# Optimization experiments

Measured on AMD Instinct MI355X. Metric: run time of the kernel, lower is better.

Reference implementation:

```python
import jax, jax.numpy as jnp
import numpy as np

INPUT_DIM = 561
NUM_CLASSES = 6
CAP_DIM = 8
NUM_CAPS = 4


def setup_inputs() -> dict:
    key = jax.random.key(0)
    ks = jax.random.split(key, 20)
    def lin(kw, kb, out_d, in_d):
        bound = 1.0 / np.sqrt(in_d)
        W = jax.random.uniform(kw, (out_d, in_d), jnp.float32, -bound, bound)
        b = jax.random.uniform(kb, (out_d,), jnp.float32, -bound, bound)
        return W, b
    x = jax.random.normal(ks[0], (65536, INPUT_DIM), jnp.float32)
    feature_weights = jnp.ones((INPUT_DIM,), jnp.float32)
    cap_W, cap_b = lin(ks[1], ks[2], NUM_CAPS * CAP_DIM, INPUT_DIM)
    q_W, q_b = lin(ks[3], ks[4], CAP_DIM, CAP_DIM)
    k_W, k_b = lin(ks[5], ks[6], CAP_DIM, CAP_DIM)
    v_W, v_b = lin(ks[7], ks[8], CAP_DIM, CAP_DIM)
    fc1_W, fc1_b = lin(ks[9], ks[10], 64, NUM_CAPS * CAP_DIM)
    fc2_W, fc2_b = lin(ks[11], ks[12], 64, 64)
    res_W, res_b = lin(ks[13], ks[14], 64, NUM_CAPS * CAP_DIM)
    out_W, out_b = lin(ks[15], ks[16], NUM_CLASSES, 64)
    return dict(x=x, feature_weights=feature_weights,
                cap_W=cap_W, cap_b=cap_b,
                q_W=q_W, q_b=q_b, k_W=k_W, k_b=k_b, v_W=v_W, v_b=v_b,
                fc1_W=fc1_W, fc1_b=fc1_b, fc2_W=fc2_W, fc2_b=fc2_b,
                res_W=res_W, res_b=res_b, out_W=out_W, out_b=out_b)


def reference(x, feature_weights, cap_W, cap_b, q_W, q_b, k_W, k_b, v_W, v_b,
              fc1_W, fc1_b, fc2_W, fc2_b, res_W, res_b, out_W, out_b):
    B = x.shape[0]
    xw = x * feature_weights
    caps = (xw @ cap_W.T + cap_b).reshape(B, NUM_CAPS, CAP_DIM)  # [B,4,8]
    Q = caps @ q_W.T + q_b
    K = caps @ k_W.T + k_b
    V = caps @ v_W.T + v_b
    scores = jnp.einsum('bqd,bkd->bqk', Q, K) / jnp.sqrt(jnp.float32(CAP_DIM))
    attn = jax.nn.softmax(scores, axis=-1)
    attended = jnp.einsum('bqk,bkd->bqd', attn, V)
    flat = attended.reshape(B, NUM_CAPS * CAP_DIM)
    res = jax.nn.relu(flat @ fc1_W.T + fc1_b)
    out = jax.nn.relu(res @ fc2_W.T + fc2_b + flat @ res_W.T + res_b)
    return out @ out_W.T + out_b
```

## Files before the change

### kernel.cpp

```cpp
#include <hip/hip_runtime.h>
#include <math.h>

#define INPUT_DIM 561
#define NCD 32

__global__ void prep_wt(const float* __restrict__ capW,
                        const float* __restrict__ fw,
                        float* __restrict__ Wt) {
    int idx = blockIdx.x * blockDim.x + threadIdx.x;
    if (idx < INPUT_DIM * NCD) {
        int k = idx >> 5;
        int c = idx & 31;
        Wt[idx] = capW[c * INPUT_DIM + k] * fw[k];
    }
}

__device__ __forceinline__ void stage16(const float* __restrict__ X,
                                        int r0, int k0, int w_s, int lane,
                                        float (*dst)[65]) {
    int kk = k0 + lane;
    if (kk > INPUT_DIM - 1) kk = INPUT_DIM - 1;
    #pragma unroll
    for (int i = 0; i < 16; ++i) {
        const int p = w_s * 16 + i;
        const float* g = X + (size_t)(r0 + p) * INPUT_DIM + kk;
        __builtin_amdgcn_global_load_lds(
            (const __attribute__((address_space(1))) void*)g,
            (__attribute__((address_space(3))) void*)&dst[p][0],
            4, 0, 0);
    }
}

__global__ void __launch_bounds__(256)
__attribute__((amdgpu_waves_per_eu(4, 4)))
caps_gemm(const float* __restrict__ X,
          const float* __restrict__ Wt,
          const float* __restrict__ cap_b,
          float* __restrict__ caps)
{
    __shared__ float smem[8448];
    float (*xb)[64][65]   = (float (*)[64][65])smem;
    float (*part)[64][33] = (float (*)[64][33])smem;

    const int tid = threadIdx.x;
    const int t   = tid & 63;
    const int w   = tid >> 6;
    const int w_s = __builtin_amdgcn_readfirstlane(w);
    const int r0  = blockIdx.x * 64;

    float acc[NCD];
    #pragma unroll
    for (int c = 0; c < NCD; ++c) acc[c] = 0.0f;

    stage16(X, r0, 0, w_s, t, xb[0]);

    const int tb = (w_s == 0) ? 0 : (13 + 12 * (w_s - 1));
    const int te = tb + ((w_s == 0) ? 13 : 12);

    int cur = 0;
    for (int ch = 0; ch < 9; ++ch) {
        asm volatile("s_waitcnt vmcnt(0)" ::: "memory");
        __syncthreads();
        const int k0 = ch * 64;
        if (ch < 8) stage16(X, r0, k0 + 64, w_s, t, xb[cur ^ 1]);

        if (ch < 8) {
            const int kb = w_s * 16;
            #pragma unroll 4
            for (int jj = 0; jj < 16; ++jj) {
                const int j = kb + jj;
                const float xv = xb[cur][t][j];
                const float* __restrict__ wrow = Wt + (size_t)(k0 + j) * NCD;
                #pragma unroll
                for (int c = 0; c < NCD; ++c)
                    acc[c] = fmaf(xv, wrow[c], acc[c]);
            }
        } else {
            for (int j = tb; j < te; ++j) {
                const float xv = xb[cur][t][j];
                const float* __restrict__ wrow = Wt + (size_t)(k0 + j) * NCD;
                #pragma unroll
                for (int c = 0; c < NCD; ++c)
                    acc[c] = fmaf(xv, wrow[c], acc[c]);
            }
        }
        cur ^= 1;
    }

    __syncthreads();
    #pragma unroll
    for (int c = 0; c < NCD; ++c) part[w][t][c] = acc[c];
    __syncthreads();
    if (w != 0) return;

    float4* __restrict__ crow = (float4*)(caps + (size_t)(r0 + t) * NCD);
    #pragma unroll
    for (int v = 0; v < 8; ++v) {
        float4 s;
        s.x = cap_b[4*v+0] + part[0][t][4*v+0] + part[1][t][4*v+0]
            + part[2][t][4*v+0] + part[3][t][4*v+0];
        s.y = cap_b[4*v+1] + part[0][t][4*v+1] + part[1][t][4*v+1]
            + part[2][t][4*v+1] + part[3][t][4*v+1];
        s.z = cap_b[4*v+2] + part[0][t][4*v+2] + part[1][t][4*v+2]
            + part[2][t][4*v+2] + part[3][t][4*v+2];
        s.w = cap_b[4*v+3] + part[0][t][4*v+3] + part[1][t][4*v+3]
            + part[2][t][4*v+3] + part[3][t][4*v+3];
        crow[v] = s;
    }
}

__device__ __forceinline__ void head_body(
    const float* __restrict__ acc,
    const float* __restrict__ qW, const float* __restrict__ qb,
    const float* __restrict__ kW, const float* __restrict__ kb,
    const float* __restrict__ vW, const float* __restrict__ vb,
    const float* __restrict__ fc1W, const float* __restrict__ fc1b,
    const float* __restrict__ fc2W, const float* __restrict__ fc2b,
    const float* __restrict__ resW, const float* __restrict__ resb,
    const float* __restrict__ outW, const float* __restrict__ outb,
    float* __restrict__ o)
{
    float Km[32], Vm[32];
    #pragma unroll
    for (int q = 0; q < 4; ++q) {
        #pragma unroll
        for (int d = 0; d < 8; ++d) {
            float ka = kb[d], va = vb[d];
            #pragma unroll
            for (int e = 0; e < 8; ++e) {
                ka = fmaf(acc[q * 8 + e], kW[d * 8 + e], ka);
                va = fmaf(acc[q * 8 + e], vW[d * 8 + e], va);
            }
            Km[q * 8 + d] = ka;
            Vm[q * 8 + d] = va;
        }
    }

    float flat[32];
    const float rs8 = 0.35355339059327373f;
    #pragma unroll
    for (int q = 0; q < 4; ++q) {
        float Q[8];
        #pragma unroll
        for (int d = 0; d < 8; ++d) {
            float a = qb[d];
            #pragma unroll
            for (int e = 0; e < 8; ++e)
                a = fmaf(acc[q * 8 + e], qW[d * 8 + e], a);
            Q[d] = a;
        }
        float sc[4];
        #pragma unroll
        for (int kq = 0; kq < 4; ++kq) {
            float a = 0.0f;
            #pragma unroll
            for (int d = 0; d < 8; ++d)
                a = fmaf(Q[d], Km[kq * 8 + d], a);
            sc[kq] = a * rs8;
        }
        const float m  = fmaxf(fmaxf(sc[0], sc[1]), fmaxf(sc[2], sc[3]));
        const float e0 = __expf(sc[0] - m);
        const float e1 = __expf(sc[1] - m);
        const float e2 = __expf(sc[2] - m);
        const float e3 = __expf(sc[3] - m);
        const float inv = 1.0f / (e0 + e1 + e2 + e3);
        #pragma unroll
        for (int d = 0; d < 8; ++d)
            flat[q * 8 + d] =
                (e0 * Vm[0 * 8 + d] + e1 * Vm[1 * 8 + d] +
                 e2 * Vm[2 * 8 + d] + e3 * Vm[3 * 8 + d]) * inv;
    }

    float res[64];
    #pragma unroll
    for (int j = 0; j < 64; ++j) {
        float a = fc1b[j];
        #pragma unroll
        for (int i = 0; i < 32; ++i)
            a = fmaf(flat[i], fc1W[j * 32 + i], a);
        res[j] = fmaxf(a, 0.0f);
    }

    #pragma unroll
    for (int p = 0; p < 6; ++p) o[p] = outb[p];
    for (int c = 0; c < 64; ++c) {
        float a = fc2b[c] + resb[c];
        #pragma unroll
        for (int j = 0; j < 64; ++j)
            a = fmaf(res[j], fc2W[c * 64 + j], a);
        #pragma unroll
        for (int i = 0; i < 32; ++i)
            a = fmaf(flat[i], resW[c * 32 + i], a);
        a = fmaxf(a, 0.0f);
        #pragma unroll
        for (int p = 0; p < 6; ++p)
            o[p] = fmaf(a, outW[p * 64 + c], o[p]);
    }
}

__global__ void __launch_bounds__(256)
__attribute__((amdgpu_waves_per_eu(1, 1)))
head_kernel(const float* __restrict__ caps,
            const float* __restrict__ qW, const float* __restrict__ qb,
            const float* __restrict__ kW, const float* __restrict__ kb,
            const float* __restrict__ vW, const float* __restrict__ vb,
            const float* __restrict__ fc1W, const float* __restrict__ fc1b,
            const float* __restrict__ fc2W, const float* __restrict__ fc2b,
            const float* __restrict__ resW, const float* __restrict__ resb,
            const float* __restrict__ outW, const float* __restrict__ outb,
            float* __restrict__ out)
{
    const int row = blockIdx.x * 256 + threadIdx.x;
    const float4* __restrict__ cp = (const float4*)(caps + (size_t)row * NCD);
    float acc[NCD];
    #pragma unroll
    for (int i = 0; i < 8; ++i) {
        const float4 v = cp[i];
        acc[4 * i + 0] = v.x; acc[4 * i + 1] = v.y;
        acc[4 * i + 2] = v.z; acc[4 * i + 3] = v.w;
    }
    float o[6];
    head_body(acc, qW, qb, kW, kb, vW, vb, fc1W, fc1b, fc2W, fc2b,
              resW, resb, outW, outb, o);
    #pragma unroll
    for (int p = 0; p < 6; ++p) out[row * 6 + p] = o[p];
}

__global__ void __launch_bounds__(256)
harcnet_fused(const float* __restrict__ X,
              const float* __restrict__ fw,
              const float* __restrict__ capW, const float* __restrict__ cap_b,
              const float* __restrict__ qW, const float* __restrict__ qb,
              const float* __restrict__ kW, const float* __restrict__ kb,
              const float* __restrict__ vW, const float* __restrict__ vb,
              const float* __restrict__ fc1W, const float* __restrict__ fc1b,
              const float* __restrict__ fc2W, const float* __restrict__ fc2b,
              const float* __restrict__ resW, const float* __restrict__ resb,
              const float* __restrict__ outW, const float* __restrict__ outb,
              float* __restrict__ out)
{
    __shared__ float part[4][64][33];
    const int t   = threadIdx.x & 63;
    const int w   = threadIdx.x >> 6;
    const int row = blockIdx.x * 64 + t;
    const float* __restrict__ Xrow = X + (size_t)row * INPUT_DIM;

    float acc[NCD];
    #pragma unroll
    for (int c = 0; c < NCD; ++c) acc[c] = 0.0f;

    const int kbeg = w * 141;
    const int kend = (kbeg + 141 < INPUT_DIM) ? kbeg + 141 : INPUT_DIM;
    for (int k = kbeg; k < kend; ++k) {
        const float xv = Xrow[k] * fw[k];
        #pragma unroll
        for (int c = 0; c < NCD; ++c)
            acc[c] = fmaf(xv, capW[c * INPUT_DIM + k], acc[c]);
    }

    #pragma unroll
    for (int c = 0; c < NCD; ++c) part[w][t][c] = acc[c];
    __syncthreads();
    if (w != 0) return;
    #pragma unroll
    for (int c = 0; c < NCD; ++c)
        acc[c] = cap_b[c] + part[0][t][c] + part[1][t][c]
                          + part[2][t][c] + part[3][t][c];
    float o[6];
    head_body(acc, qW, qb, kW, kb, vW, vb, fc1W, fc1b, fc2W, fc2b,
              resW, resb, outW, outb, o);
    #pragma unroll
    for (int p = 0; p < 6; ++p) out[row * 6 + p] = o[p];
}

extern "C" void kernel_launch(void* const* d_in, const int* in_sizes, int n_in,
                              void* d_out, int out_size, void* d_ws, size_t ws_size,
                              hipStream_t stream) {
    const float* X     = (const float*)d_in[0];
    const float* fw    = (const float*)d_in[1];
    const float* capW  = (const float*)d_in[2];
    const float* cap_b = (const float*)d_in[3];
    const float* qW    = (const float*)d_in[4];
    const float* qb    = (const float*)d_in[5];
    const float* kW    = (const float*)d_in[6];
    const float* kb    = (const float*)d_in[7];
    const float* vW    = (const float*)d_in[8];
    const float* vb    = (const float*)d_in[9];
    const float* fc1W  = (const float*)d_in[10];
    const float* fc1b  = (const float*)d_in[11];
    const float* fc2W  = (const float*)d_in[12];
    const float* fc2b  = (const float*)d_in[13];
    const float* resW  = (const float*)d_in[14];
    const float* resb  = (const float*)d_in[15];
    const float* outW  = (const float*)d_in[16];
    const float* outb  = (const float*)d_in[17];
    float* out = (float*)d_out;

    const int nrows = in_sizes[0] / INPUT_DIM;
    const size_t caps_off   = 73728;
    const size_t caps_bytes = (size_t)nrows * NCD * sizeof(float);

    float* Wt   = (float*)d_ws;
    float* caps = (float*)((char*)d_ws + caps_off);

    if (ws_size >= caps_off + caps_bytes) {
        prep_wt<<<(INPUT_DIM * NCD + 255) / 256, 256, 0, stream>>>(capW, fw, Wt);
        caps_gemm<<<nrows / 64, 256, 0, stream>>>(X, Wt, cap_b, caps);
        head_kernel<<<nrows / 256, 256, 0, stream>>>(
            caps, qW, qb, kW, kb, vW, vb, fc1W, fc1b, fc2W, fc2b,
            resW, resb, outW, outb, out);
    } else {
        harcnet_fused<<<nrows / 64, 256, 0, stream>>>(
            X, fw, capW, cap_b, qW, qb, kW, kb, vW, vb,
            fc1W, fc1b, fc2W, fc2b, resW, resb, outW, outb, out);
    }
}
```

Before: 382.7 us.

## Split head MLP across 4 threads per row with packed LDS weights

The head kernel now assigns four threads to each row. Each thread computes 16 of the fc1 outputs and 16 of the fc2 outputs, gathers the full fc1 result through shuffles, and the six output logits are reduced with xor shuffles. All head weights are packed into one workspace buffer by a new pack kernel and staged into LDS per block, and occupancy hints move from 1 to 3-4 waves per EU. This is meant to cut the per-thread register pressure and serial work of the previous one-row-per-thread head, which ran at one wave per EU. In exchange the attention part is recomputed redundantly by all four threads and an extra small kernel launch is added. The caps GEMM inner loop also preloads 16 LDS values before the FMA loop.

Result: faster. 332.6 us (-13.1%).

```diff
diff --git a/kernel.cpp b/kernel.cpp
--- a/kernel.cpp
+++ b/kernel.cpp
@@ -3,6 +3,22 @@
 
 #define INPUT_DIM 561
 #define NCD 32
+
+#define QW   0
+#define QB   64
+#define KW   72
+#define KB   136
+#define VW   144
+#define VB   208
+#define FC1W 216
+#define FC1B 2264
+#define FC2W 2328
+#define FC2B 6424
+#define RESW 6488
+#define RESB 8536
+#define OUTW 8600
+#define OUTB 8984
+#define HW_N 8990
 
 __global__ void prep_wt(const float* __restrict__ capW,
                         const float* __restrict__ fw,
@@ -13,6 +29,34 @@
         int c = idx & 31;
         Wt[idx] = capW[c * INPUT_DIM + k] * fw[k];
     }
+}
+
+__global__ void pack_hw(const float* __restrict__ qW, const float* __restrict__ qb,
+                        const float* __restrict__ kW, const float* __restrict__ kb,
+                        const float* __restrict__ vW, const float* __restrict__ vb,
+                        const float* __restrict__ fc1W, const float* __restrict__ fc1b,
+                        const float* __restrict__ fc2W, const float* __restrict__ fc2b,
+                        const float* __restrict__ resW, const float* __restrict__ resb,
+                        const float* __restrict__ outW, const float* __restrict__ outb,
+                        float* __restrict__ hw) {
+    int i = blockIdx.x * blockDim.x + threadIdx.x;
+    if (i >= HW_N) return;
+    float v;
+    if      (i < QB)   v = qW[i - QW];
+    else if (i < KW)   v = qb[i - QB];
+    else if (i < KB)   v = kW[i - KW];
+    else if (i < VW)   v = kb[i - KB];
+    else if (i < VB)   v = vW[i - VW];
+    else if (i < FC1W) v = vb[i - VB];
+    else if (i < FC1B) v = fc1W[i - FC1W];
+    else if (i < FC2W) v = fc1b[i - FC1B];
+    else if (i < FC2B) v = fc2W[i - FC2W];
+    else if (i < RESW) v = fc2b[i - FC2B];
+    else if (i < RESB) v = resW[i - RESW];
+    else if (i < OUTW) v = resb[i - RESB];
+    else if (i < OUTB) v = outW[i - OUTW];
+    else               v = outb[i - OUTB];
+    hw[i] = v;
 }
 
 __device__ __forceinline__ void stage16(const float* __restrict__ X,
@@ -66,14 +110,16 @@
 
         if (ch < 8) {
             const int kb = w_s * 16;
-            #pragma unroll 4
+            float xv[16];
+            #pragma unroll
+            for (int jj = 0; jj < 16; ++jj)
+                xv[jj] = xb[cur][t][kb + jj];
+            #pragma unroll
             for (int jj = 0; jj < 16; ++jj) {
-                const int j = kb + jj;
-                const float xv = xb[cur][t][j];
-                const float* __restrict__ wrow = Wt + (size_t)(k0 + j) * NCD;
+                const float* __restrict__ wrow = Wt + (size_t)(k0 + kb + jj) * NCD;
                 #pragma unroll
                 for (int c = 0; c < NCD; ++c)
-                    acc[c] = fmaf(xv, wrow[c], acc[c]);
+                    acc[c] = fmaf(xv[jj], wrow[c], acc[c]);
             }
         } else {
             for (int j = tb; j < te; ++j) {
@@ -109,30 +155,42 @@
     }
 }
 
-__device__ __forceinline__ void head_body(
-    const float* __restrict__ acc,
-    const float* __restrict__ qW, const float* __restrict__ qb,
-    const float* __restrict__ kW, const float* __restrict__ kb,
-    const float* __restrict__ vW, const float* __restrict__ vb,
-    const float* __restrict__ fc1W, const float* __restrict__ fc1b,
-    const float* __restrict__ fc2W, const float* __restrict__ fc2b,
-    const float* __restrict__ resW, const float* __restrict__ resb,
-    const float* __restrict__ outW, const float* __restrict__ outb,
-    float* __restrict__ o)
+__global__ void __launch_bounds__(256)
+__attribute__((amdgpu_waves_per_eu(3, 4)))
+head_kernel(const float* __restrict__ caps,
+            const float* __restrict__ hwg,
+            float* __restrict__ out)
 {
+    __shared__ float hw[HW_N];
+    const int tid = threadIdx.x;
+    for (int i = tid; i < HW_N; i += 256) hw[i] = hwg[i];
+    __syncthreads();
+
+    const int g    = tid & 3;
+    const int row  = blockIdx.x * 64 + (tid >> 2);
+    const int lane = tid & 63;
+
+    const float4* __restrict__ cp = (const float4*)(caps + (size_t)row * NCD);
+    float acc[NCD];
+    #pragma unroll
+    for (int i = 0; i < 8; ++i) {
+        const float4 v = cp[i];
+        acc[4*i+0] = v.x; acc[4*i+1] = v.y; acc[4*i+2] = v.z; acc[4*i+3] = v.w;
+    }
+
     float Km[32], Vm[32];
     #pragma unroll
     for (int q = 0; q < 4; ++q) {
         #pragma unroll
         for (int d = 0; d < 8; ++d) {
-            float ka = kb[d], va = vb[d];
+            float ka = hw[KB + d], va = hw[VB + d];
             #pragma unroll
             for (int e = 0; e < 8; ++e) {
-                ka = fmaf(acc[q * 8 + e], kW[d * 8 + e], ka);
-                va = fmaf(acc[q * 8 + e], vW[d * 8 + e], va);
+                ka = fmaf(acc[q*8+e], hw[KW + d*8+e], ka);
+                va = fmaf(acc[q*8+e], hw[VW + d*8+e], va);
             }
-            Km[q * 8 + d] = ka;
-            Vm[q * 8 + d] = va;
+            Km[q*8+d] = ka;
+            Vm[q*8+d] = va;
         }
     }
 
@@ -143,10 +201,10 @@
         float Q[8];
         #pragma unroll
         for (int d = 0; d < 8; ++d) {
-            float a = qb[d];
+            float a = hw[QB + d];
             #pragma unroll
             for (int e = 0; e < 8; ++e)
-                a = fmaf(acc[q * 8 + e], qW[d * 8 + e], a);
+                a = fmaf(acc[q*8+e], hw[QW + d*8+e], a);
             Q[d] = a;
         }
         float sc[4];
@@ -155,75 +213,70 @@
             float a = 0.0f;
             #pragma unroll
             for (int d = 0; d < 8; ++d)
-                a = fmaf(Q[d], Km[kq * 8 + d], a);
+                a = fmaf(Q[d], Km[kq*8+d], a);
             sc[kq] = a * rs8;
         }
         const float m  = fmaxf(fmaxf(sc[0], sc[1]), fmaxf(sc[2], sc[3]));
-        const float e0 = __expf(sc[0] - m);
-        const float e1 = __expf(sc[1] - m);
-        const float e2 = __expf(sc[2] - m);
-        const float e3 = __expf(sc[3] - m);
-        const float inv = 1.0f / (e0 + e1 + e2 + e3);
+        const float e0 = __expf(sc[0]-m), e1 = __expf(sc[1]-m);
+        const float e2 = __expf(sc[2]-m), e3 = __expf(sc[3]-m);
+        const float inv = 1.0f / (e0+e1+e2+e3);
         #pragma unroll
         for (int d = 0; d < 8; ++d)
-            flat[q * 8 + d] =
-                (e0 * Vm[0 * 8 + d] + e1 * Vm[1 * 8 + d] +
-                 e2 * Vm[2 * 8 + d] + e3 * Vm[3 * 8 + d]) * inv;
-    }
-
-    float res[64];
-    #pragma unroll
-    for (int j = 0; j < 64; ++j) {
-        float a = fc1b[j];
+            flat[q*8+d] = (e0*Vm[0*8+d] + e1*Vm[1*8+d] +
+                           e2*Vm[2*8+d] + e3*Vm[3*8+d]) * inv;
+    }
+
+    const int j0 = g * 16;
+    float res_[16];
+    #pragma unroll
+    for (int jj = 0; jj < 16; ++jj) {
+        const int j = j0 + jj;
+        float a = hw[FC1B + j];
         #pragma unroll
         for (int i = 0; i < 32; ++i)
-            a = fmaf(flat[i], fc1W[j * 32 + i], a);
-        res[j] = fmaxf(a, 0.0f);
-    }
-
-    #pragma unroll
-    for (int p = 0; p < 6; ++p) o[p] = outb[p];
-    for (int c = 0; c < 64; ++c) {
-        float a = fc2b[c] + resb[c];
+            a = fmaf(flat[i], hw[FC1W + j*32 + i], a);
+        res_[jj] = fmaxf(a, 0.0f);
+    }
+
+    float res_full[64];
+    const int lbase = lane & ~3;
+    #pragma unroll
+    for (int gg = 0; gg < 4; ++gg) {
+        #pragma unroll
+        for (int jj = 0; jj < 16; ++jj)
+            res_full[gg*16 + jj] = __shfl(res_[jj], lbase | gg, 64);
+    }
+
+    float o[6];
+    #pragma unroll
+    for (int p = 0; p < 6; ++p) o[p] = 0.0f;
+
+    #pragma unroll 2
+    for (int cc = 0; cc < 16; ++cc) {
+        const int c = j0 + cc;
+        float s = hw[FC2B + c] + hw[RESB + c];
         #pragma unroll
         for (int j = 0; j < 64; ++j)
-            a = fmaf(res[j], fc2W[c * 64 + j], a);
+            s = fmaf(res_full[j], hw[FC2W + c*64 + j], s);
         #pragma unroll
         for (int i = 0; i < 32; ++i)
-            a = fmaf(flat[i], resW[c * 32 + i], a);
-        a = fmaxf(a, 0.0f);
+            s = fmaf(flat[i], hw[RESW + c*32 + i], s);
+        s = fmaxf(s, 0.0f);
         #pragma unroll
         for (int p = 0; p < 6; ++p)
-            o[p] = fmaf(a, outW[p * 64 + c], o[p]);
-    }
-}
-
-__global__ void __launch_bounds__(256)
-__attribute__((amdgpu_waves_per_eu(1, 1)))
-head_kernel(const float* __restrict__ caps,
-            const float* __restrict__ qW, const float* __restrict__ qb,
-            const float* __restrict__ kW, const float* __restrict__ kb,
-            const float* __restrict__ vW, const float* __restrict__ vb,
-            const float* __restrict__ fc1W, const float* __restrict__ fc1b,
-            const float* __restrict__ fc2W, const float* __restrict__ fc2b,
-            const float* __restrict__ resW, const float* __restrict__ resb,
-            const float* __restrict__ outW, const float* __restrict__ outb,
-            float* __restrict__ out)
-{
-    const int row = blockIdx.x * 256 + threadIdx.x;
-    const float4* __restrict__ cp = (const float4*)(caps + (size_t)row * NCD);
-    float acc[NCD];
-    #pragma unroll
-    for (int i = 0; i < 8; ++i) {
-        const float4 v = cp[i];
-        acc[4 * i + 0] = v.x; acc[4 * i + 1] = v.y;
-        acc[4 * i + 2] = v.z; acc[4 * i + 3] = v.w;
-    }
-    float o[6];
-    head_body(acc, qW, qb, kW, kb, vW, vb, fc1W, fc1b, fc2W, fc2b,
-              resW, resb, outW, outb, o);
-    #pragma unroll
-    for (int p = 0; p < 6; ++p) out[row * 6 + p] = o[p];
+            o[p] = fmaf(s, hw[OUTW + p*64 + c], o[p]);
+    }
+
+    #pragma unroll
+    for (int p = 0; p < 6; ++p) {
+        o[p] += __shfl_xor(o[p], 1, 64);
+        o[p] += __shfl_xor(o[p], 2, 64);
+    }
+    if (g == 0) {
+        #pragma unroll
+        for (int p = 0; p < 6; ++p)
+            out[row*6 + p] = o[p] + hw[OUTB + p];
+    }
 }
 
 __global__ void __launch_bounds__(256)
@@ -266,11 +319,71 @@
     for (int c = 0; c < NCD; ++c)
         acc[c] = cap_b[c] + part[0][t][c] + part[1][t][c]
                           + part[2][t][c] + part[3][t][c];
+
+    float Km[32], Vm[32];
+    #pragma unroll
+    for (int q = 0; q < 4; ++q)
+        #pragma unroll
+        for (int d = 0; d < 8; ++d) {
+            float ka = kb[d], va = vb[d];
+            #pragma unroll
+            for (int e = 0; e < 8; ++e) {
+                ka = fmaf(acc[q*8+e], kW[d*8+e], ka);
+                va = fmaf(acc[q*8+e], vW[d*8+e], va);
+            }
+            Km[q*8+d] = ka; Vm[q*8+d] = va;
+        }
+    float flat[32];
+    const float rs8 = 0.35355339059327373f;
+    #pragma unroll
+    for (int q = 0; q < 4; ++q) {
+        float Q[8];
+        #pragma unroll
+        for (int d = 0; d < 8; ++d) {
+            float a = qb[d];
+            #pragma unroll
+            for (int e = 0; e < 8; ++e) a = fmaf(acc[q*8+e], qW[d*8+e], a);
+            Q[d] = a;
+        }
+        float sc[4];
+        #pragma unroll
+        for (int kq = 0; kq < 4; ++kq) {
+            float a = 0.0f;
+            #pragma unroll
+            for (int d = 0; d < 8; ++d) a = fmaf(Q[d], Km[kq*8+d], a);
+            sc[kq] = a * rs8;
+        }
+        const float m  = fmaxf(fmaxf(sc[0], sc[1]), fmaxf(sc[2], sc[3]));
+        const float e0 = __expf(sc[0]-m), e1 = __expf(sc[1]-m);
+        const float e2 = __expf(sc[2]-m), e3 = __expf(sc[3]-m);
+        const float inv = 1.0f / (e0+e1+e2+e3);
+        #pragma unroll
+        for (int d = 0; d < 8; ++d)
+            flat[q*8+d] = (e0*Vm[0*8+d]+e1*Vm[1*8+d]+e2*Vm[2*8+d]+e3*Vm[3*8+d])*inv;
+    }
+    float res[64];
+    #pragma unroll
+    for (int j = 0; j < 64; ++j) {
+        float a = fc1b[j];
+        #pragma unroll
+        for (int i = 0; i < 32; ++i) a = fmaf(flat[i], fc1W[j*32+i], a);
+        res[j] = fmaxf(a, 0.0f);
+    }
     float o[6];
-    head_body(acc, qW, qb, kW, kb, vW, vb, fc1W, fc1b, fc2W, fc2b,
-              resW, resb, outW, outb, o);
-    #pragma unroll
-    for (int p = 0; p < 6; ++p) out[row * 6 + p] = o[p];
+    #pragma unroll
+    for (int p = 0; p < 6; ++p) o[p] = outb[p];
+    for (int c = 0; c < 64; ++c) {
+        float a = fc2b[c] + resb[c];
+        #pragma unroll
+        for (int j = 0; j < 64; ++j) a = fmaf(res[j], fc2W[c*64+j], a);
+        #pragma unroll
+        for (int i = 0; i < 32; ++i) a = fmaf(flat[i], resW[c*32+i], a);
+        a = fmaxf(a, 0.0f);
+        #pragma unroll
+        for (int p = 0; p < 6; ++p) o[p] = fmaf(a, outW[p*64+c], o[p]);
+    }
+    #pragma unroll
+    for (int p = 0; p < 6; ++p) out[row*6+p] = o[p];
 }
 
 extern "C" void kernel_launch(void* const* d_in, const int* in_sizes, int n_in,
@@ -297,18 +410,21 @@
     float* out = (float*)d_out;
 
     const int nrows = in_sizes[0] / INPUT_DIM;
-    const size_t caps_off   = 73728;
+    const size_t hw_off     = 73728;
+    const size_t caps_off   = 110592;
     const size_t caps_bytes = (size_t)nrows * NCD * sizeof(float);
 
     float* Wt   = (float*)d_ws;
+    float* hw   = (float*)((char*)d_ws + hw_off);
     float* caps = (float*)((char*)d_ws + caps_off);
 
     if (ws_size >= caps_off + caps_bytes) {
         prep_wt<<<(INPUT_DIM * NCD + 255) / 256, 256, 0, stream>>>(capW, fw, Wt);
+        pack_hw<<<(HW_N + 255) / 256, 256, 0, stream>>>(
+            qW, qb, kW, kb, vW, vb, fc1W, fc1b, fc2W, fc2b,
+            resW, resb, outW, outb, hw);
         caps_gemm<<<nrows / 64, 256, 0, stream>>>(X, Wt, cap_b, caps);
-        head_kernel<<<nrows / 256, 256, 0, stream>>>(
-            caps, qW, qb, kW, kb, vW, vb, fc1W, fc1b, fc2W, fc2b,
-            resW, resb, outW, outb, out);
+        head_kernel<<<nrows / 64, 256, 0, stream>>>(caps, hw, out);
     } else {
         harcnet_fused<<<nrows / 64, 256, 0, stream>>>(
             X, fw, capW, cap_b, qW, qb, kW, kb, vW, vb,
```
